# Kernel optimization log

Measured on AMD Instinct MI355X. Metric: run time of the kernel, lower is better.

The kernel has to match this reference:

```python
import jax, jax.numpy as jnp
import numpy as np

B, V, K, D, E, NE = 32, 512, 16, 128, 32, 8192


def setup_inputs() -> dict:
    key = jax.random.key(0)
    ks = jax.random.split(key, 12)
    s = 0.05
    return {
        "vertex_features": jax.random.normal(ks[0], (B, V, D), jnp.float32),
        "atom_adj": jax.random.randint(ks[1], (B * V * K,), 0, B * V),
        "bond_adj": jax.random.randint(ks[2], (B * V * K,), 0, B * NE),
        "h0": jax.random.normal(ks[3], (B, V, D), jnp.float32),
        "lamda": jnp.full((1,), 0.5, jnp.float32),
        "alpha": jnp.full((1,), 0.1, jnp.float32),
        "l": 1,
        "edge_initial": jax.random.normal(ks[4], (B, NE, E), jnp.float32),
        "vertex_mask": jnp.ones((B, V), jnp.float32),
        "nbs_mask": jax.random.uniform(ks[5], (B, V, K), jnp.float32),
        # label_U1: (D+E) -> D ; label_U2: 2D -> D ; feature_updating: D -> D (variant=False)
        "W1": jax.random.normal(ks[6], (D, D + E), jnp.float32) * s,
        "b1": jax.random.normal(ks[7], (D,), jnp.float32) * s,
        "W2": jax.random.normal(ks[8], (D, 2 * D), jnp.float32) * s,
        "b2": jax.random.normal(ks[9], (D,), jnp.float32) * s,
        "W3": jax.random.normal(ks[10], (D, D), jnp.float32) * s,
        "b3": jax.random.normal(ks[11], (D,), jnp.float32) * s,
    }


def reference(vertex_features, atom_adj, bond_adj, h0, lamda, alpha, l,
              edge_initial, vertex_mask, nbs_mask, W1, b1, W2, b2, W3, b3):
    b, v = vertex_mask.shape
    k = nbs_mask.shape[2]
    d = vertex_features.shape[-1]
    e = edge_initial.shape[-1]
    # gather neighbor vertex and edge features (flat index, torch.index_select semantics)
    vn = vertex_features.reshape(-1, d)[atom_adj].reshape(b, v, k, d)
    en = edge_initial.reshape(-1, e)[bond_adj].reshape(b, v, k, e)
    l_neighbor = jnp.concatenate([vn, en], axis=-1)            # [b,v,k,d+e]
    nl = jax.nn.gelu(l_neighbor @ W1.T + b1, approximate=False)  # exact GELU like torch F.gelu
    nl = jnp.sum(nl * nbs_mask[..., None], axis=-2)            # masked sum over neighbors -> [b,v,d]
    hi = jnp.concatenate([nl, vertex_features], axis=-1) @ W2.T + b2
    theta = jnp.log(lamda / l + 1.0)                           # broadcast scalar (shape [1])
    support = (1.0 - alpha) * hi + alpha * h0                  # variant=False: r == support
    out = theta * (support @ W3.T + b3) + (1.0 - theta) * support
    out = out + vertex_features                                # residual=True
    return out
```

## Files before the change

kernel.cpp:

```cpp
#include <hip/hip_runtime.h>
#include <hip/hip_bf16.h>
#include <math.h>

#define NLSTR 136
#define ASTR  168

typedef __bf16 bf16x8 __attribute__((ext_vector_type(8)));
typedef float f32x4 __attribute__((ext_vector_type(4)));
typedef float f32x16 __attribute__((ext_vector_type(16)));
typedef unsigned short ushort8v __attribute__((ext_vector_type(8)));

union FragU { ushort8v u; bf16x8 b; };

static __device__ inline unsigned short f2bf(float f){
  unsigned u = __float_as_uint(f);
  u += 0x7fffu + ((u >> 16) & 1u);
  return (unsigned short)(u >> 16);
}
static __device__ inline unsigned pk2(float a, float b){
  union { __hip_bfloat162 h; unsigned u; } r;
  r.h = __float22bfloat162_rn(float2{a, b});
  return r.u;
}
static __device__ inline ushort8v pkcvt8(float4 a, float4 b){
  union { unsigned u[4]; ushort8v v; } r;
  r.u[0] = pk2(a.x, a.y); r.u[1] = pk2(a.z, a.w);
  r.u[2] = pk2(b.x, b.y); r.u[3] = pk2(b.z, b.w);
  return r.v;
}

static __device__ inline float gelu_f(float x){
  float u = x * x;
  float p = fmaf(u, -0.1029434273f, -2.3022084765f);
  float e = __builtin_amdgcn_exp2f(x * p);
  return x * __builtin_amdgcn_rcpf(1.0f + e);
}

#define WG_BARRIER() asm volatile("s_waitcnt lgkmcnt(0)\n\ts_barrier" ::: "memory")

__global__ __launch_bounds__(256) void prep_kernel(
    const float* __restrict__ vf, const float* __restrict__ W1,
    const float* __restrict__ W2, const float* __restrict__ W3,
    unsigned short* __restrict__ vfbf, unsigned short* __restrict__ w1f,
    unsigned short* __restrict__ w2f, unsigned short* __restrict__ w3f)
{
  int t = blockIdx.x * 256 + threadIdx.x;
  if (t < 262144){
    const float4* src = (const float4*)vf;
    float4 x = src[t * 2], y = src[t * 2 + 1];
    *(ushort8v*)(vfbf + t * 8) = pkcvt8(x, y);
    return;
  }
  int t2 = t - 262144;
  const float* s;
  unsigned short* d;
  if (t2 < 2560){
    int fragid = t2 >> 6, lane = t2 & 63;
    int nc2 = fragid / 10, kc = fragid % 10, n = lane & 31, h = lane >> 5;
    s = W1 + (nc2 * 32 + n) * 160 + kc * 16 + h * 8;
    d = w1f + t2 * 8;
  } else if (t2 < 6656){
    int t3 = t2 - 2560;
    int fragid = t3 >> 6, lane = t3 & 63;
    int kc = fragid >> 3, nc = fragid & 7, col = lane & 15, quad = lane >> 4;
    s = W2 + (nc * 16 + col) * 256 + kc * 32 + quad * 8;
    d = w2f + t3 * 8;
  } else if (t2 < 8704){
    int t3 = t2 - 6656;
    int fragid = t3 >> 6, lane = t3 & 63;
    int kc = fragid >> 3, nc = fragid & 7, col = lane & 15, quad = lane >> 4;
    s = W3 + (nc * 16 + col) * 128 + kc * 32 + quad * 8;
    d = w3f + t3 * 8;
  } else return;
#pragma unroll
  for (int j = 0; j < 8; j++) d[j] = f2bf(s[j]);
}

__global__ __launch_bounds__(256, 3) void fused_kernel(
    const unsigned short* __restrict__ vfbf,
    const float* __restrict__ vf,
    const int* __restrict__ aadj, const int* __restrict__ badj,
    const float* __restrict__ edge, const float* __restrict__ nbs,
    const float* __restrict__ h0,
    const unsigned short* __restrict__ w1f, const unsigned short* __restrict__ w2f,
    const unsigned short* __restrict__ w3f,
    const float* __restrict__ b1, const float* __restrict__ b2, const float* __restrict__ b3,
    const float* __restrict__ lamda, const float* __restrict__ alpha,
    const int* __restrict__ lval,
    float* __restrict__ out)
{
  __shared__ __align__(16) unsigned short abuf[4][32 * ASTR];
  __shared__ __align__(16) unsigned short nl_lds[16 * NLSTR];
  __shared__ __align__(16) unsigned short sup_lds[16 * NLSTR];
  __shared__ __align__(16) float nbs_lds[256];
  const int wid  = threadIdx.x >> 6;
  const int lane = threadIdx.x & 63;
  const int n32  = lane & 31;
  const int h    = lane >> 5;
  const int col  = lane & 15;
  const int quad = lane >> 4;
  const int v0   = blockIdx.x * 16;

  const int srow = threadIdx.x >> 3;
  const int ssub = threadIdx.x & 7;

  float4 wu[10];
  {
    const float4* vsrc = (const float4*)vfbf;
    const int vb = (blockIdx.x >> 3) * 2048 + threadIdx.x;
#pragma unroll
    for (int i = 0; i < 8; i++) wu[i] = vsrc[vb + i * 256];
    const float4* esrc = (const float4*)edge;
    const int eb = (blockIdx.x >> 3) * 512 + threadIdx.x;
    wu[8] = esrc[eb]; wu[9] = esrc[eb + 256];
  }

  nbs_lds[threadIdx.x] = nbs[v0 * 16 + threadIdx.x];

  int a_all[8], e_all[8];
  {
    const int base = (v0 + (srow >> 4)) * 16 + (srow & 15);
#pragma unroll
    for (int p = 0; p < 8; p++){
      a_all[p] = aadj[base + 32 * p];
      e_all[p] = badj[base + 32 * p];
    }
  }

#pragma unroll
  for (int i = 0; i < 10; i++)
    asm volatile("" :: "v"(wu[i].x), "v"(wu[i].y), "v"(wu[i].z), "v"(wu[i].w));

  ushort8v sv[4][2]; float4 se[4];
#pragma unroll
  for (int q = 0; q < 4; q++){
    const ushort8v* vs = (const ushort8v*)(vfbf + (size_t)a_all[q] * 128 + ssub * 16);
    sv[q][0] = vs[0]; sv[q][1] = vs[1];
    se[q] = *(const float4*)(edge + (size_t)e_all[q] * 32 + ssub * 4);
  }

  FragU bw[10];
#pragma unroll
  for (int kc = 0; kc < 10; kc++)
    bw[kc].u = *(const ushort8v*)(w1f + ((wid * 10 + kc) * 64 + lane) * 8);

  const float bb1 = b1[wid * 32 + n32];

#pragma unroll
  for (int q = 0; q < 4; q++){
    unsigned short* dst = abuf[q] + srow * ASTR + ssub * 16;
    *(ushort8v*)dst = sv[q][0]; *(ushort8v*)(dst + 8) = sv[q][1];
    unsigned* ed = (unsigned*)(abuf[q] + srow * ASTR + 128 + ssub * 4);
    ed[0] = pk2(se[q].x, se[q].y); ed[1] = pk2(se[q].z, se[q].w);
  }
  WG_BARRIER();

#pragma unroll
  for (int q = 0; q < 4; q++){
    const ushort8v* vs = (const ushort8v*)(vfbf + (size_t)a_all[q + 4] * 128 + ssub * 16);
    sv[q][0] = vs[0]; sv[q][1] = vs[1];
    se[q] = *(const float4*)(edge + (size_t)e_all[q + 4] * 32 + ssub * 4);
  }

  const float4* nbsl = (const float4*)nbs_lds;

#pragma unroll
  for (int p = 0; p < 4; p++){
    const float4 mAlo = nbsl[8 * p + h],     mAhi = nbsl[8 * p + 2 + h];
    const float4 mBlo = nbsl[8 * p + 4 + h], mBhi = nbsl[8 * p + 6 + h];
    const unsigned short* ab = abuf[p] + n32 * ASTR + h * 8;
    f32x16 acc;
#pragma unroll
    for (int j = 0; j < 16; j++) acc[j] = bb1;
#pragma unroll
    for (int kc = 0; kc < 10; kc++){
      FragU fa;
      fa.u = *(const ushort8v*)(ab + kc * 16);
      acc = __builtin_amdgcn_mfma_f32_32x32x16_bf16(fa.b, bw[kc].b, acc, 0, 0, 0);
    }
    float sA = fmaf(gelu_f(acc[0]),  mAlo.x, gelu_f(acc[1])  * mAlo.y)
             + fmaf(gelu_f(acc[2]),  mAlo.z, gelu_f(acc[3])  * mAlo.w)
             + fmaf(gelu_f(acc[4]),  mAhi.x, gelu_f(acc[5])  * mAhi.y)
             + fmaf(gelu_f(acc[6]),  mAhi.z, gelu_f(acc[7])  * mAhi.w);
    float sB = fmaf(gelu_f(acc[8]),  mBlo.x, gelu_f(acc[9])  * mBlo.y)
             + fmaf(gelu_f(acc[10]), mBlo.z, gelu_f(acc[11]) * mBlo.w)
             + fmaf(gelu_f(acc[12]), mBhi.x, gelu_f(acc[13]) * mBhi.y)
             + fmaf(gelu_f(acc[14]), mBhi.z, gelu_f(acc[15]) * mBhi.w);
    sA += __shfl_xor(sA, 32, 64);
    sB += __shfl_xor(sB, 32, 64);
    if (h == 0) nl_lds[(2 * p)     * NLSTR + wid * 32 + n32] = f2bf(sA);
    else        nl_lds[(2 * p + 1) * NLSTR + wid * 32 + n32] = f2bf(sB);
  }
  WG_BARRIER();

#pragma unroll
  for (int q = 0; q < 4; q++){
    unsigned short* dst = abuf[q] + srow * ASTR + ssub * 16;
    *(ushort8v*)dst = sv[q][0]; *(ushort8v*)(dst + 8) = sv[q][1];
    unsigned* ed = (unsigned*)(abuf[q] + srow * ASTR + 128 + ssub * 4);
    ed[0] = pk2(se[q].x, se[q].y); ed[1] = pk2(se[q].z, se[q].w);
  }
  WG_BARRIER();

#pragma unroll
  for (int p = 0; p < 4; p++){
    const int pp = p + 4;
    const float4 mAlo = nbsl[8 * pp + h],     mAhi = nbsl[8 * pp + 2 + h];
    const float4 mBlo = nbsl[8 * pp + 4 + h], mBhi = nbsl[8 * pp + 6 + h];
    const unsigned short* ab = abuf[p] + n32 * ASTR + h * 8;
    f32x16 acc;
#pragma unroll
    for (int j = 0; j < 16; j++) acc[j] = bb1;
#pragma unroll
    for (int kc = 0; kc < 10; kc++){
      FragU fa;
      fa.u = *(const ushort8v*)(ab + kc * 16);
      acc = __builtin_amdgcn_mfma_f32_32x32x16_bf16(fa.b, bw[kc].b, acc, 0, 0, 0);
    }
    float sA = fmaf(gelu_f(acc[0]),  mAlo.x, gelu_f(acc[1])  * mAlo.y)
             + fmaf(gelu_f(acc[2]),  mAlo.z, gelu_f(acc[3])  * mAlo.w)
             + fmaf(gelu_f(acc[4]),  mAhi.x, gelu_f(acc[5])  * mAhi.y)
             + fmaf(gelu_f(acc[6]),  mAhi.z, gelu_f(acc[7])  * mAhi.w);
    float sB = fmaf(gelu_f(acc[8]),  mBlo.x, gelu_f(acc[9])  * mBlo.y)
             + fmaf(gelu_f(acc[10]), mBlo.z, gelu_f(acc[11]) * mBlo.w)
             + fmaf(gelu_f(acc[12]), mBhi.x, gelu_f(acc[13]) * mBhi.y)
             + fmaf(gelu_f(acc[14]), mBhi.z, gelu_f(acc[15]) * mBhi.w);
    sA += __shfl_xor(sA, 32, 64);
    sB += __shfl_xor(sB, 32, 64);
    if (h == 0) nl_lds[(2 * pp)     * NLSTR + wid * 32 + n32] = f2bf(sA);
    else        nl_lds[(2 * pp + 1) * NLSTR + wid * 32 + n32] = f2bf(sB);
  }
  __syncthreads();

  const int nc0 = 2 * wid;
  const float th = logf(lamda[0] / (float)lval[0] + 1.0f);
  const float al = alpha[0];

  float h0v[2][4];
#pragma unroll
  for (int pq = 0; pq < 2; pq++){
    const int d = (nc0 + pq) * 16 + col;
#pragma unroll
    for (int r = 0; r < 4; r++)
      h0v[pq][r] = h0[(v0 + quad * 4 + r) * 128 + d];
  }

  f32x4 acc2[2] = {};
#pragma unroll
  for (int kc = 0; kc < 8; kc++){
    FragU a;
    if (kc < 4) a.u = *(const ushort8v*)(nl_lds + col * NLSTR + kc * 32 + quad * 8);
    else        a.u = *(const ushort8v*)(vfbf + (size_t)(v0 + col) * 128 + (kc - 4) * 32 + quad * 8);
#pragma unroll
    for (int pq = 0; pq < 2; pq++){
      FragU bf_;
      bf_.u = *(const ushort8v*)(w2f + ((kc * 8 + nc0 + pq) * 64 + lane) * 8);
      acc2[pq] = __builtin_amdgcn_mfma_f32_16x16x32_bf16(a.b, bf_.b, acc2[pq], 0, 0, 0);
    }
  }

  float sup[2][4];
#pragma unroll
  for (int pq = 0; pq < 2; pq++){
    const int d = (nc0 + pq) * 16 + col;
    const float bb = b2[d];
#pragma unroll
    for (int r = 0; r < 4; r++){
      float hi = acc2[pq][r] + bb;
      float s = (1.f - al) * hi + al * h0v[pq][r];
      sup[pq][r] = s;
      sup_lds[(quad * 4 + r) * NLSTR + d] = f2bf(s);
    }
  }
  __syncthreads();

  float rv[2][4];
#pragma unroll
  for (int pq = 0; pq < 2; pq++){
    const int d = (nc0 + pq) * 16 + col;
#pragma unroll
    for (int r = 0; r < 4; r++)
      rv[pq][r] = vf[(size_t)(v0 + quad * 4 + r) * 128 + d];
  }

  f32x4 acc3[2] = {};
#pragma unroll
  for (int kc = 0; kc < 4; kc++){
    FragU a;
    a.u = *(const ushort8v*)(sup_lds + col * NLSTR + kc * 32 + quad * 8);
#pragma unroll
    for (int pq = 0; pq < 2; pq++){
      FragU bf_;
      bf_.u = *(const ushort8v*)(w3f + ((kc * 8 + nc0 + pq) * 64 + lane) * 8);
      acc3[pq] = __builtin_amdgcn_mfma_f32_16x16x32_bf16(a.b, bf_.b, acc3[pq], 0, 0, 0);
    }
  }

#pragma unroll
  for (int pq = 0; pq < 2; pq++){
    const int d = (nc0 + pq) * 16 + col;
    const float bb = b3[d];
#pragma unroll
    for (int r = 0; r < 4; r++){
      const int vtx = v0 + quad * 4 + r;
      out[vtx * 128 + d] = th * (acc3[pq][r] + bb) + (1.f - th) * sup[pq][r] + rv[pq][r];
    }
  }
}

extern "C" void kernel_launch(void* const* d_in, const int* in_sizes, int n_in,
                              void* d_out, int out_size, void* d_ws, size_t ws_size,
                              hipStream_t stream)
{
  const float* vfp  = (const float*)d_in[0];
  const int*   aadj = (const int*)d_in[1];
  const int*   badj = (const int*)d_in[2];
  const float* h0   = (const float*)d_in[3];
  const float* lam  = (const float*)d_in[4];
  const float* alp  = (const float*)d_in[5];
  const int*   lv   = (const int*)d_in[6];
  const float* edge = (const float*)d_in[7];
  const float* nbs  = (const float*)d_in[9];
  const float* W1   = (const float*)d_in[10];
  const float* b1   = (const float*)d_in[11];
  const float* W2   = (const float*)d_in[12];
  const float* b2   = (const float*)d_in[13];
  const float* W3   = (const float*)d_in[14];
  const float* b3   = (const float*)d_in[15];
  float* out = (float*)d_out;

  unsigned short* w1f  = (unsigned short*)d_ws;
  unsigned short* w2f  = w1f + 20480;
  unsigned short* w3f  = w2f + 32768;
  unsigned short* vfbf = w3f + 16384;

  prep_kernel<<<1058, 256, 0, stream>>>(vfp, W1, W2, W3, vfbf, w1f, w2f, w3f);
  fused_kernel<<<1024, 256, 0, stream>>>(vfbf, vfp, aadj, badj, edge, nbs, h0,
                                         w1f, w2f, w3f, b1, b2, b3, lam, alp, lv, out);
}
```

Before: 136.2 us.

## Pre-convert edge features to bf16 and gather bf16 edges in fused kernel

Extends the prep kernel to convert the whole edge_initial tensor to bf16 in workspace when the workspace is large enough. The fused kernel is templated so it can gather bf16 edge rows directly instead of gathering fp32 rows and packing them. The aim is to halve the bytes moved by the random edge gather. It also removes the early vertex/edge prefetch loads, and it reads the residual vertex features from the bf16 copy instead of fp32. In exchange it adds a full read and write pass over the large edge tensor every call, and the bf16 residual lowers output precision.

```diff
diff --git a/kernel.cpp b/kernel.cpp
--- a/kernel.cpp
+++ b/kernel.cpp
@@ -9,6 +9,7 @@
 typedef float f32x4 __attribute__((ext_vector_type(4)));
 typedef float f32x16 __attribute__((ext_vector_type(16)));
 typedef unsigned short ushort8v __attribute__((ext_vector_type(8)));
+typedef unsigned short ushort4v __attribute__((ext_vector_type(4)));
 
 union FragU { ushort8v u; bf16x8 b; };
 
@@ -16,6 +17,9 @@
   unsigned u = __float_as_uint(f);
   u += 0x7fffu + ((u >> 16) & 1u);
   return (unsigned short)(u >> 16);
+}
+static __device__ inline float bf2f(unsigned short u){
+  return __uint_as_float(((unsigned)u) << 16);
 }
 static __device__ inline unsigned pk2(float a, float b){
   union { __hip_bfloat162 h; unsigned u; } r;
@@ -41,8 +45,10 @@
 __global__ __launch_bounds__(256) void prep_kernel(
     const float* __restrict__ vf, const float* __restrict__ W1,
     const float* __restrict__ W2, const float* __restrict__ W3,
+    const float* __restrict__ edge,
     unsigned short* __restrict__ vfbf, unsigned short* __restrict__ w1f,
-    unsigned short* __restrict__ w2f, unsigned short* __restrict__ w3f)
+    unsigned short* __restrict__ w2f, unsigned short* __restrict__ w3f,
+    unsigned short* __restrict__ edgebf)
 {
   int t = blockIdx.x * 256 + threadIdx.x;
   if (t < 262144){
@@ -52,6 +58,15 @@
     return;
   }
   int t2 = t - 262144;
+  if (t2 >= 8704){
+    int t3 = t2 - 8704;
+    if (t3 < 1048576 && edgebf){
+      const float4* src = (const float4*)edge;
+      float4 x = src[t3 * 2], y = src[t3 * 2 + 1];
+      *(ushort8v*)(edgebf + t3 * 8) = pkcvt8(x, y);
+    }
+    return;
+  }
   const float* s;
   unsigned short* d;
   if (t2 < 2560){
@@ -65,23 +80,23 @@
     int kc = fragid >> 3, nc = fragid & 7, col = lane & 15, quad = lane >> 4;
     s = W2 + (nc * 16 + col) * 256 + kc * 32 + quad * 8;
     d = w2f + t3 * 8;
-  } else if (t2 < 8704){
+  } else {
     int t3 = t2 - 6656;
     int fragid = t3 >> 6, lane = t3 & 63;
     int kc = fragid >> 3, nc = fragid & 7, col = lane & 15, quad = lane >> 4;
     s = W3 + (nc * 16 + col) * 128 + kc * 32 + quad * 8;
     d = w3f + t3 * 8;
-  } else return;
+  }
 #pragma unroll
   for (int j = 0; j < 8; j++) d[j] = f2bf(s[j]);
 }
 
+template<bool EBF>
 __global__ __launch_bounds__(256, 3) void fused_kernel(
     const unsigned short* __restrict__ vfbf,
-    const float* __restrict__ vf,
     const int* __restrict__ aadj, const int* __restrict__ badj,
-    const float* __restrict__ edge, const float* __restrict__ nbs,
-    const float* __restrict__ h0,
+    const unsigned short* __restrict__ edgebf, const float* __restrict__ edge,
+    const float* __restrict__ nbs, const float* __restrict__ h0,
     const unsigned short* __restrict__ w1f, const unsigned short* __restrict__ w2f,
     const unsigned short* __restrict__ w3f,
     const float* __restrict__ b1, const float* __restrict__ b2, const float* __restrict__ b3,
@@ -104,17 +119,6 @@
   const int srow = threadIdx.x >> 3;
   const int ssub = threadIdx.x & 7;
 
-  float4 wu[10];
-  {
-    const float4* vsrc = (const float4*)vfbf;
-    const int vb = (blockIdx.x >> 3) * 2048 + threadIdx.x;
-#pragma unroll
-    for (int i = 0; i < 8; i++) wu[i] = vsrc[vb + i * 256];
-    const float4* esrc = (const float4*)edge;
-    const int eb = (blockIdx.x >> 3) * 512 + threadIdx.x;
-    wu[8] = esrc[eb]; wu[9] = esrc[eb + 256];
-  }
-
   nbs_lds[threadIdx.x] = nbs[v0 * 16 + threadIdx.x];
 
   int a_all[8], e_all[8];
@@ -127,16 +131,13 @@
     }
   }
 
-#pragma unroll
-  for (int i = 0; i < 10; i++)
-    asm volatile("" :: "v"(wu[i].x), "v"(wu[i].y), "v"(wu[i].z), "v"(wu[i].w));
-
-  ushort8v sv[4][2]; float4 se[4];
+  ushort8v sv[4][2]; ushort4v seb[4]; float4 sef[4];
 #pragma unroll
   for (int q = 0; q < 4; q++){
     const ushort8v* vs = (const ushort8v*)(vfbf + (size_t)a_all[q] * 128 + ssub * 16);
     sv[q][0] = vs[0]; sv[q][1] = vs[1];
-    se[q] = *(const float4*)(edge + (size_t)e_all[q] * 32 + ssub * 4);
+    if (EBF) seb[q] = *(const ushort4v*)(edgebf + (size_t)e_all[q] * 32 + ssub * 4);
+    else     sef[q] = *(const float4*)(edge + (size_t)e_all[q] * 32 + ssub * 4);
   }
 
   FragU bw[10];
@@ -150,8 +151,12 @@
   for (int q = 0; q < 4; q++){
     unsigned short* dst = abuf[q] + srow * ASTR + ssub * 16;
     *(ushort8v*)dst = sv[q][0]; *(ushort8v*)(dst + 8) = sv[q][1];
-    unsigned* ed = (unsigned*)(abuf[q] + srow * ASTR + 128 + ssub * 4);
-    ed[0] = pk2(se[q].x, se[q].y); ed[1] = pk2(se[q].z, se[q].w);
+    if (EBF){
+      *(ushort4v*)(abuf[q] + srow * ASTR + 128 + ssub * 4) = seb[q];
+    } else {
+      unsigned* ed = (unsigned*)(abuf[q] + srow * ASTR + 128 + ssub * 4);
+      ed[0] = pk2(sef[q].x, sef[q].y); ed[1] = pk2(sef[q].z, sef[q].w);
+    }
   }
   WG_BARRIER();
 
@@ -159,7 +164,8 @@
   for (int q = 0; q < 4; q++){
     const ushort8v* vs = (const ushort8v*)(vfbf + (size_t)a_all[q + 4] * 128 + ssub * 16);
     sv[q][0] = vs[0]; sv[q][1] = vs[1];
-    se[q] = *(const float4*)(edge + (size_t)e_all[q + 4] * 32 + ssub * 4);
+    if (EBF) seb[q] = *(const ushort4v*)(edgebf + (size_t)e_all[q + 4] * 32 + ssub * 4);
+    else     sef[q] = *(const float4*)(edge + (size_t)e_all[q + 4] * 32 + ssub * 4);
   }
 
   const float4* nbsl = (const float4*)nbs_lds;
@@ -197,8 +203,12 @@
   for (int q = 0; q < 4; q++){
     unsigned short* dst = abuf[q] + srow * ASTR + ssub * 16;
     *(ushort8v*)dst = sv[q][0]; *(ushort8v*)(dst + 8) = sv[q][1];
-    unsigned* ed = (unsigned*)(abuf[q] + srow * ASTR + 128 + ssub * 4);
-    ed[0] = pk2(se[q].x, se[q].y); ed[1] = pk2(se[q].z, se[q].w);
+    if (EBF){
+      *(ushort4v*)(abuf[q] + srow * ASTR + 128 + ssub * 4) = seb[q];
+    } else {
+      unsigned* ed = (unsigned*)(abuf[q] + srow * ASTR + 128 + ssub * 4);
+      ed[0] = pk2(sef[q].x, sef[q].y); ed[1] = pk2(sef[q].z, sef[q].w);
+    }
   }
   WG_BARRIER();
 
@@ -280,7 +290,7 @@
     const int d = (nc0 + pq) * 16 + col;
 #pragma unroll
     for (int r = 0; r < 4; r++)
-      rv[pq][r] = vf[(size_t)(v0 + quad * 4 + r) * 128 + d];
+      rv[pq][r] = bf2f(vfbf[(size_t)(v0 + quad * 4 + r) * 128 + d]);
   }
 
   f32x4 acc3[2] = {};
@@ -329,12 +339,25 @@
   const float* b3   = (const float*)d_in[15];
   float* out = (float*)d_out;
 
-  unsigned short* w1f  = (unsigned short*)d_ws;
-  unsigned short* w2f  = w1f + 20480;
-  unsigned short* w3f  = w2f + 32768;
-  unsigned short* vfbf = w3f + 16384;
-
-  prep_kernel<<<1058, 256, 0, stream>>>(vfp, W1, W2, W3, vfbf, w1f, w2f, w3f);
-  fused_kernel<<<1024, 256, 0, stream>>>(vfbf, vfp, aadj, badj, edge, nbs, h0,
-                                         w1f, w2f, w3f, b1, b2, b3, lam, alp, lv, out);
-}
+  unsigned short* w1f    = (unsigned short*)d_ws;
+  unsigned short* w2f    = w1f + 20480;
+  unsigned short* w3f    = w2f + 32768;
+  unsigned short* vfbf   = w3f + 16384;
+  unsigned short* edgebf = vfbf + 2097152;
+
+  const bool ebf = ws_size >= (size_t)(2166784 + 8388608) * sizeof(unsigned short);
+
+  if (ebf){
+    prep_kernel<<<5154, 256, 0, stream>>>(vfp, W1, W2, W3, edge,
+                                          vfbf, w1f, w2f, w3f, edgebf);
+    fused_kernel<true><<<1024, 256, 0, stream>>>(vfbf, aadj, badj, edgebf, edge,
+                                                 nbs, h0, w1f, w2f, w3f,
+                                                 b1, b2, b3, lam, alp, lv, out);
+  } else {
+    prep_kernel<<<1058, 256, 0, stream>>>(vfp, W1, W2, W3, edge,
+                                          vfbf, w1f, w2f, w3f, (unsigned short*)nullptr);
+    fused_kernel<false><<<1024, 256, 0, stream>>>(vfbf, aadj, badj, edgebf, edge,
+                                                  nbs, h0, w1f, w2f, w3f,
+                                                  b1, b2, b3, lam, alp, lv, out);
+  }
+}
```

After: 138.3 us. About the same (+1.6%).
